# Kernel tuning notes

Hardware: AMD Instinct MI355X
Metric: run time of the kernel (lower is better)

Reference implementation:

```python
import jax, jax.numpy as jnp
import numpy as np

B, N, C = 8, 100000, 64  # replicas, atoms, constraints


def setup_inputs() -> dict:
    key = jax.random.key(0)
    k1, k2, k3 = jax.random.split(key, 3)
    mom = jax.random.normal(k1, (B, N, 3), dtype=jnp.float32)
    # masses strictly positive
    mas = jax.random.uniform(k2, (B, N), dtype=jnp.float32, minval=0.5, maxval=1.5)
    dtm = jnp.full((B,), 1e-3, dtype=jnp.float32)  # timestep per replica
    jac_con_pos = jax.random.normal(k3, (B, C, N, 3), dtype=jnp.float32) * 0.1
    bme_lmd_tmp = jnp.zeros((B, C), dtype=jnp.float32)
    return {"mom": mom, "mas": mas, "dtm": dtm,
            "jac_con_pos": jac_con_pos, "bme_lmd_tmp": bme_lmd_tmp}


def reference(mom, mas, dtm, jac_con_pos, bme_lmd_tmp):
    # RATTLE momentum projection. rattle_objective is linear in lmd:
    #   dot(lmd) = b - dtm * G @ lmd,  G = J M^-1 J^T,  b = J M^-1 p
    # so the torch Newton loop converges exactly in one step to
    #   lmd = solve(dtm * G, b).
    inv_mas = 1.0 / mas                                   # [B,N]
    wjac = jac_con_pos * inv_mas[:, None, :, None]        # J M^-1, [B,C,N,3]
    b = jnp.einsum('bcnd,bnd->bc', wjac, mom)             # [B,C]
    G = jnp.einsum('bcnd,bknd->bck', wjac, jac_con_pos)   # [B,C,C]
    A = dtm[:, None, None] * G                            # Newton Jacobian (negated)
    lmd = jnp.linalg.solve(A, b[:, :, None])[:, :, 0]     # [B,C]
    frc = -jnp.einsum('bc,bcnd->bnd', lmd, jac_con_pos)   # constraint force
    mom_out = mom + frc * dtm[:, None, None]
    return mom_out, bme_lmd_tmp + lmd
```

## Files before the change

### kernel.cpp

```cpp
#include <hip/hip_runtime.h>

#define B_ 8
#define N_ 100000
#define C_ 64
#define K_ 300000
#define K4_ (K_/4)
#define AP_BLK ((K4_ + 255)/256)

#define KB 128
#define TILES ((K_ + KB - 1)/KB)
#define P1B 128
#define P1Q (TILES/P1B)
#define P1R (TILES%P1B)

typedef __attribute__((ext_vector_type(8))) short short8;
typedef __attribute__((ext_vector_type(4))) float f32x4;

__device__ __forceinline__ unsigned int f2bf(float x) {
    union { float f; unsigned int u; } v; v.f = x;
    unsigned int r = v.u + 0x7FFFu + ((v.u >> 16) & 1u);
    return r >> 16;
}

__global__ __launch_bounds__(256) void prep_kernel(
    const float* __restrict__ mas, const float* __restrict__ mom,
    float* __restrict__ wk, float* __restrict__ smom,
    float* __restrict__ zbuf, int nzero)
{
    const int i = blockIdx.x*256 + threadIdx.x;
    if (i < nzero) zbuf[i] = 0.0f;
    if (i < B_*K4_) {
        const int b  = i / K4_;
        const int k4 = i - b*K4_;
        const int k  = 4*k4;
        const float* mb = mas + (size_t)b*N_;
        float4 w;
        w.x = rsqrtf(mb[(k+0)/3]);
        w.y = rsqrtf(mb[(k+1)/3]);
        w.z = rsqrtf(mb[(k+2)/3]);
        w.w = rsqrtf(mb[(k+3)/3]);
        const float4 p = ((const float4*)(mom + (size_t)b*K_))[k4];
        float4 s; s.x = p.x*w.x; s.y = p.y*w.y; s.z = p.z*w.z; s.w = p.w*w.w;
        ((float4*)(wk   + (size_t)b*K_))[k4] = w;
        ((float4*)(smom + (size_t)b*K_))[k4] = s;
    }
}

__global__ __launch_bounds__(256) void pass1_mfma(
    const float* __restrict__ jac, const float* __restrict__ wk,
    const float* __restrict__ smom, float* __restrict__ Gws, float* __restrict__ bws)
{
    __shared__ __align__(16) unsigned short sbf[64*KB];

    const int b    = blockIdx.x / P1B;
    const int blk  = blockIdx.x % P1B;
    const int tid  = threadIdx.x;
    const int lane = tid & 63;
    const int wv   = tid >> 6;
    const int g    = tid & 15;
    const int r0   = tid >> 4;
    const int lrow = lane & 15;
    const int lkg  = lane >> 4;

    const float* jacb = jac  + (size_t)b * C_ * K_;
    const float* wkb  = wk   + (size_t)b * K_;
    const float* smb  = smom + (size_t)b * K_;

    const int start = blk*P1Q + (blk < P1R ? blk : P1R);
    const int cnt   = P1Q + (blk < P1R ? 1 : 0);

    f32x4 acc[4] = {{0.f,0.f,0.f,0.f},{0.f,0.f,0.f,0.f},{0.f,0.f,0.f,0.f},{0.f,0.f,0.f,0.f}};
    float bacc[4] = {0.f, 0.f, 0.f, 0.f};

    for (int t = 0; t < cnt; ++t) {
        const int k0 = (start + t) * KB;
        const int kb = k0 + g*8;
        __syncthreads();

        if (kb < K_) {
            const float4 w0 = *(const float4*)&wkb[kb];
            const float4 w1 = *(const float4*)&wkb[kb + 4];
            const float4 m0 = *(const float4*)&smb[kb];
            const float4 m1 = *(const float4*)&smb[kb + 4];
            #pragma unroll
            for (int i = 0; i < 4; ++i) {
                const int r = r0 + 16*i;
                const float4 a0 = *(const float4*)&jacb[(size_t)r*K_ + kb];
                const float4 a1 = *(const float4*)&jacb[(size_t)r*K_ + kb + 4];
                const float s0 = a0.x*w0.x, s1 = a0.y*w0.y, s2 = a0.z*w0.z, s3 = a0.w*w0.w;
                const float s4 = a1.x*w1.x, s5 = a1.y*w1.y, s6 = a1.z*w1.z, s7 = a1.w*w1.w;
                bacc[i] += s0*m0.x + s1*m0.y + s2*m0.z + s3*m0.w
                         + s4*m1.x + s5*m1.y + s6*m1.z + s7*m1.w;
                uint4 pk;
                pk.x = (f2bf(s1) << 16) | f2bf(s0);
                pk.y = (f2bf(s3) << 16) | f2bf(s2);
                pk.z = (f2bf(s5) << 16) | f2bf(s4);
                pk.w = (f2bf(s7) << 16) | f2bf(s6);
                *(uint4*)&sbf[r*KB + ((g ^ (r & 15)) * 8)] = pk;
            }
        } else {
            const uint4 pk = make_uint4(0u,0u,0u,0u);
            #pragma unroll
            for (int i = 0; i < 4; ++i) {
                const int r = r0 + 16*i;
                *(uint4*)&sbf[r*KB + ((g ^ (r & 15)) * 8)] = pk;
            }
        }
        __syncthreads();

        const int ra = wv*16 + lrow;
        #pragma unroll
        for (int q = 0; q < 4; ++q) {
            const int ga = (q*4 + lkg) ^ (ra & 15);
            const short8 af = *(const short8*)&sbf[ra*KB + ga*8];
            #pragma unroll
            for (int p = 0; p < 4; ++p) {
                const int rb = p*16 + lrow;
                const int gb = (q*4 + lkg) ^ (rb & 15);
                const short8 bf = *(const short8*)&sbf[rb*KB + gb*8];
                acc[p] = __builtin_amdgcn_mfma_f32_16x16x32_bf16(af, bf, acc[p], 0, 0, 0);
            }
        }
    }

    float* Gb = Gws + b*4096;
    #pragma unroll
    for (int p = 0; p < 4; ++p) {
        #pragma unroll
        for (int reg = 0; reg < 4; ++reg) {
            const int row = 16*wv + lkg*4 + reg;
            const int col = 16*p + lrow;
            atomicAdd(&Gb[row*64 + col], acc[p][reg]);
        }
    }
    #pragma unroll
    for (int i = 0; i < 4; ++i) {
        float v = bacc[i];
        v += __shfl_xor(v, 1);
        v += __shfl_xor(v, 2);
        v += __shfl_xor(v, 4);
        v += __shfl_xor(v, 8);
        if ((tid & 15) == 0) atomicAdd(&bws[b*64 + r0 + 16*i], v);
    }
}

__global__ __launch_bounds__(256) void solve_kernel(
    const float* __restrict__ Gws, const float* __restrict__ bws,
    const float* __restrict__ dtm, const float* __restrict__ bme,
    float* __restrict__ lmd_ws, float* __restrict__ out_lmd)
{
    __shared__ float A[64*65];
    __shared__ float lmd_s[64];
    const int b = blockIdx.x;
    const int tid = threadIdx.x;
    const float dt = dtm[b];
    const float* Gb = Gws + b*4096;

    for (int e = tid; e < 64*65; e += 256) {
        int j = e / 65, k = e % 65;
        A[e] = (k < 64) ? dt * Gb[j*64 + k] : bws[b*64 + j];
    }
    __syncthreads();

    const int row = tid & 63;
    const int cg  = tid >> 6;
    for (int i = 0; i < 64; i++) {
        float f = 0.0f;
        if (row > i) f = A[row*65 + i] / A[i*65 + i];
        int k0 = i + 1;
        k0 += (cg - k0) & 3;
        if (row > i) {
            for (int k = k0; k <= 64; k += 4)
                A[row*65 + k] -= f * A[i*65 + k];
        }
        __syncthreads();
    }

    for (int i = 63; i >= 0; i--) {
        if (tid == i) lmd_s[i] = A[i*65 + 64] / A[i*65 + i];
        __syncthreads();
        if (tid < i) A[tid*65 + 64] -= A[tid*65 + i] * lmd_s[i];
        __syncthreads();
    }

    if (tid < 64) {
        float l = lmd_s[tid];
        lmd_ws[b*64 + tid] = l;
        out_lmd[b*64 + tid] = bme[b*64 + tid] + l;
    }
}

__global__ __launch_bounds__(256) void apply_kernel(
    const float* __restrict__ jac, const float* __restrict__ mom,
    const float* __restrict__ dtm, const float* __restrict__ lmd_ws,
    float* __restrict__ out)
{
    __shared__ float ls[64];
    const int b   = blockIdx.x / AP_BLK;
    const int blk = blockIdx.x % AP_BLK;
    if (threadIdx.x < 64) ls[threadIdx.x] = lmd_ws[b*64 + threadIdx.x] * dtm[b];
    __syncthreads();
    const int k4 = blk*256 + threadIdx.x;
    if (k4 >= K4_) return;

    const float4* jb = (const float4*)(jac + (size_t)b * C_ * K_);
    float4 a = make_float4(0.f, 0.f, 0.f, 0.f);
    #pragma unroll 8
    for (int c = 0; c < 64; c++) {
        float4 v = jb[(size_t)c * K4_ + k4];
        float l = ls[c];
        a.x -= l*v.x; a.y -= l*v.y; a.z -= l*v.z; a.w -= l*v.w;
    }
    const float4 m = ((const float4*)(mom + (size_t)b * K_))[k4];
    float4 o;
    o.x = m.x + a.x; o.y = m.y + a.y; o.z = m.z + a.z; o.w = m.w + a.w;
    ((float4*)out)[(size_t)b * K4_ + k4] = o;
}

extern "C" void kernel_launch(void* const* d_in, const int* in_sizes, int n_in,
                              void* d_out, int out_size, void* d_ws, size_t ws_size,
                              hipStream_t stream) {
    const float* mom = (const float*)d_in[0];
    const float* mas = (const float*)d_in[1];
    const float* dtm = (const float*)d_in[2];
    const float* jac = (const float*)d_in[3];
    const float* bme = (const float*)d_in[4];
    float* out = (float*)d_out;

    float* Gws    = (float*)d_ws;
    float* bws    = Gws + B_*4096;
    float* lmd_ws = bws + B_*64;
    float* wk     = lmd_ws + B_*64;
    float* smom   = wk + (size_t)B_*K_;

    const int nzero = B_*4096 + B_*64;
    prep_kernel<<<(B_*K4_ + 255)/256, 256, 0, stream>>>(mas, mom, wk, smom, Gws, nzero);
    pass1_mfma<<<B_*P1B, 256, 0, stream>>>(jac, wk, smom, Gws, bws);
    solve_kernel<<<B_, 256, 0, stream>>>(Gws, bws, dtm, bme, lmd_ws, out + (size_t)B_*K_);
    apply_kernel<<<B_*AP_BLK, 256, 0, stream>>>(jac, mom, dtm, lmd_ws, out);
}
```

Measured before the change: 325.3 us.

## Feed MFMA operands directly from global memory, dropping the LDS staging

The Gram-matrix pass no longer stages bf16-converted Jacobian tiles in shared memory. Each wave now loads its own A rows and all 64 B rows straight from global memory and converts them to bf16 in registers, which removes both block barriers per tile. Tiles are handed out to blocks in a strided pattern instead of contiguous ranges. The catch is that the four waves of a block each reload and reconvert the same B rows, so cache traffic and conversion ALU work grow about fourfold, and the per-lane loads are less coalesced.

```diff
diff --git a/kernel.cpp b/kernel.cpp
--- a/kernel.cpp
+++ b/kernel.cpp
@@ -10,8 +10,6 @@
 #define KB 128
 #define TILES ((K_ + KB - 1)/KB)
 #define P1B 128
-#define P1Q (TILES/P1B)
-#define P1R (TILES%P1B)
 
 typedef __attribute__((ext_vector_type(8))) short short8;
 typedef __attribute__((ext_vector_type(4))) float f32x4;
@@ -50,15 +48,11 @@
     const float* __restrict__ jac, const float* __restrict__ wk,
     const float* __restrict__ smom, float* __restrict__ Gws, float* __restrict__ bws)
 {
-    __shared__ __align__(16) unsigned short sbf[64*KB];
-
     const int b    = blockIdx.x / P1B;
     const int blk  = blockIdx.x % P1B;
     const int tid  = threadIdx.x;
     const int lane = tid & 63;
     const int wv   = tid >> 6;
-    const int g    = tid & 15;
-    const int r0   = tid >> 4;
     const int lrow = lane & 15;
     const int lkg  = lane >> 4;
 
@@ -66,60 +60,54 @@
     const float* wkb  = wk   + (size_t)b * K_;
     const float* smb  = smom + (size_t)b * K_;
 
-    const int start = blk*P1Q + (blk < P1R ? blk : P1R);
-    const int cnt   = P1Q + (blk < P1R ? 1 : 0);
+    const float* rowA = jacb + (size_t)(wv*16 + lrow) * K_;
+    const float* rowB0 = jacb + (size_t)(lrow) * K_;
 
     f32x4 acc[4] = {{0.f,0.f,0.f,0.f},{0.f,0.f,0.f,0.f},{0.f,0.f,0.f,0.f},{0.f,0.f,0.f,0.f}};
-    float bacc[4] = {0.f, 0.f, 0.f, 0.f};
-
-    for (int t = 0; t < cnt; ++t) {
-        const int k0 = (start + t) * KB;
-        const int kb = k0 + g*8;
-        __syncthreads();
-
-        if (kb < K_) {
-            const float4 w0 = *(const float4*)&wkb[kb];
-            const float4 w1 = *(const float4*)&wkb[kb + 4];
-            const float4 m0 = *(const float4*)&smb[kb];
-            const float4 m1 = *(const float4*)&smb[kb + 4];
-            #pragma unroll
-            for (int i = 0; i < 4; ++i) {
-                const int r = r0 + 16*i;
-                const float4 a0 = *(const float4*)&jacb[(size_t)r*K_ + kb];
-                const float4 a1 = *(const float4*)&jacb[(size_t)r*K_ + kb + 4];
-                const float s0 = a0.x*w0.x, s1 = a0.y*w0.y, s2 = a0.z*w0.z, s3 = a0.w*w0.w;
-                const float s4 = a1.x*w1.x, s5 = a1.y*w1.y, s6 = a1.z*w1.z, s7 = a1.w*w1.w;
-                bacc[i] += s0*m0.x + s1*m0.y + s2*m0.z + s3*m0.w
-                         + s4*m1.x + s5*m1.y + s6*m1.z + s7*m1.w;
-                uint4 pk;
-                pk.x = (f2bf(s1) << 16) | f2bf(s0);
-                pk.y = (f2bf(s3) << 16) | f2bf(s2);
-                pk.z = (f2bf(s5) << 16) | f2bf(s4);
-                pk.w = (f2bf(s7) << 16) | f2bf(s6);
-                *(uint4*)&sbf[r*KB + ((g ^ (r & 15)) * 8)] = pk;
-            }
-        } else {
-            const uint4 pk = make_uint4(0u,0u,0u,0u);
-            #pragma unroll
-            for (int i = 0; i < 4; ++i) {
-                const int r = r0 + 16*i;
-                *(uint4*)&sbf[r*KB + ((g ^ (r & 15)) * 8)] = pk;
-            }
-        }
-        __syncthreads();
-
-        const int ra = wv*16 + lrow;
-        #pragma unroll
-        for (int q = 0; q < 4; ++q) {
-            const int ga = (q*4 + lkg) ^ (ra & 15);
-            const short8 af = *(const short8*)&sbf[ra*KB + ga*8];
+    float bacc = 0.f;
+
+    for (int tile = blk; tile < TILES; tile += P1B) {
+        const int k0   = tile * KB;
+        const int kmax = K_ - k0;
+        const int kb   = k0 + lkg*8;
+
+        auto qstep = [&](int q) {
+            const int kq = kb + q*32;
+            const float4 w0 = *(const float4*)&wkb[kq];
+            const float4 w1 = *(const float4*)&wkb[kq + 4];
+            const float4 a0 = *(const float4*)&rowA[kq];
+            const float4 a1 = *(const float4*)&rowA[kq + 4];
+            const float4 m0 = *(const float4*)&smb[kq];
+            const float4 m1 = *(const float4*)&smb[kq + 4];
+            const float s0 = a0.x*w0.x, s1 = a0.y*w0.y, s2 = a0.z*w0.z, s3 = a0.w*w0.w;
+            const float s4 = a1.x*w1.x, s5 = a1.y*w1.y, s6 = a1.z*w1.z, s7 = a1.w*w1.w;
+            bacc += s0*m0.x + s1*m0.y + s2*m0.z + s3*m0.w
+                  + s4*m1.x + s5*m1.y + s6*m1.z + s7*m1.w;
+            short8 af;
+            ((unsigned int*)&af)[0] = (f2bf(s1) << 16) | f2bf(s0);
+            ((unsigned int*)&af)[1] = (f2bf(s3) << 16) | f2bf(s2);
+            ((unsigned int*)&af)[2] = (f2bf(s5) << 16) | f2bf(s4);
+            ((unsigned int*)&af)[3] = (f2bf(s7) << 16) | f2bf(s6);
             #pragma unroll
             for (int p = 0; p < 4; ++p) {
-                const int rb = p*16 + lrow;
-                const int gb = (q*4 + lkg) ^ (rb & 15);
-                const short8 bf = *(const short8*)&sbf[rb*KB + gb*8];
+                const float* rowB = rowB0 + (size_t)p*16*K_;
+                const float4 b0 = *(const float4*)&rowB[kq];
+                const float4 b1 = *(const float4*)&rowB[kq + 4];
+                const float t0 = b0.x*w0.x, t1 = b0.y*w0.y, t2 = b0.z*w0.z, t3 = b0.w*w0.w;
+                const float t4 = b1.x*w1.x, t5 = b1.y*w1.y, t6 = b1.z*w1.z, t7 = b1.w*w1.w;
+                short8 bf;
+                ((unsigned int*)&bf)[0] = (f2bf(t1) << 16) | f2bf(t0);
+                ((unsigned int*)&bf)[1] = (f2bf(t3) << 16) | f2bf(t2);
+                ((unsigned int*)&bf)[2] = (f2bf(t5) << 16) | f2bf(t4);
+                ((unsigned int*)&bf)[3] = (f2bf(t7) << 16) | f2bf(t6);
                 acc[p] = __builtin_amdgcn_mfma_f32_16x16x32_bf16(af, bf, acc[p], 0, 0, 0);
             }
+        };
+
+        if (kmax >= KB) {
+            qstep(0); qstep(1); qstep(2); qstep(3);
+        } else {
+            for (int q = 0; q*32 < kmax; ++q) qstep(q);
         }
     }
 
@@ -133,15 +121,9 @@
             atomicAdd(&Gb[row*64 + col], acc[p][reg]);
         }
     }
-    #pragma unroll
-    for (int i = 0; i < 4; ++i) {
-        float v = bacc[i];
-        v += __shfl_xor(v, 1);
-        v += __shfl_xor(v, 2);
-        v += __shfl_xor(v, 4);
-        v += __shfl_xor(v, 8);
-        if ((tid & 15) == 0) atomicAdd(&bws[b*64 + r0 + 16*i], v);
-    }
+    bacc += __shfl_xor(bacc, 16);
+    bacc += __shfl_xor(bacc, 32);
+    if (lkg == 0) atomicAdd(&bws[b*64 + wv*16 + lrow], bacc);
 }
 
 __global__ __launch_bounds__(256) void solve_kernel(
```

After: 563.0 us. 1.73x slower.
